# Performance work log

Measured on AMD Instinct MI355X. Metric: run time of the kernel, lower is better.

The kernel has to match this reference:

```python
import jax, jax.numpy as jnp
import numpy as np

N = 100000        # num nodes
E = 800000        # num edges
N_T = 1
IN_FEATS = 128
NUM_HEAD = 8
O_FEATS = 16
O_HEAD = NUM_HEAD * O_FEATS  # 128
LN_EPS = 1e-5


def setup_inputs() -> dict:
    key = jax.random.key(0)
    ks = [jax.random.fold_in(key, i) for i in range(16)]
    feats = jax.random.normal(ks[0], (N, N_T, IN_FEATS), dtype=jnp.float32)
    edge_src = jax.random.randint(ks[1], (E,), 0, N, dtype=jnp.int32)
    # ensure every node has at least one incoming edge (avoids 0/0 in wv/z)
    dst_rest = jax.random.randint(ks[2], (E - N,), 0, N, dtype=jnp.int32)
    edge_dst = jax.random.permutation(ks[3], jnp.concatenate([jnp.arange(N, dtype=jnp.int32), dst_rest]))
    s_in = 1.0 / np.sqrt(IN_FEATS)
    s_oh = 1.0 / np.sqrt(O_HEAD)
    Wq = jax.random.normal(ks[4], (IN_FEATS, O_HEAD), dtype=jnp.float32) * s_in
    bq = jnp.zeros((O_HEAD,), dtype=jnp.float32)
    Wk = jax.random.normal(ks[5], (IN_FEATS, O_HEAD), dtype=jnp.float32) * s_in
    bk = jnp.zeros((O_HEAD,), dtype=jnp.float32)
    Wv = jax.random.normal(ks[6], (IN_FEATS, O_HEAD), dtype=jnp.float32) * s_in
    bv = jnp.zeros((O_HEAD,), dtype=jnp.float32)
    Wo = jax.random.normal(ks[7], (O_HEAD, O_HEAD), dtype=jnp.float32) * s_oh
    bo = jnp.zeros((O_HEAD,), dtype=jnp.float32)
    Wffn = jax.random.normal(ks[8], (IN_FEATS, O_HEAD), dtype=jnp.float32) * s_in
    bffn = jnp.zeros((O_HEAD,), dtype=jnp.float32)
    ln_g = jnp.ones((O_HEAD,), dtype=jnp.float32)
    ln_b = jnp.zeros((O_HEAD,), dtype=jnp.float32)
    return {"feats": feats, "edge_src": edge_src, "edge_dst": edge_dst,
            "Wq": Wq, "bq": bq, "Wk": Wk, "bk": bk, "Wv": Wv, "bv": bv,
            "Wo": Wo, "bo": bo, "Wffn": Wffn, "bffn": bffn,
            "ln_g": ln_g, "ln_b": ln_b}


def _layer_norm(x, g, b):
    mu = jnp.mean(x, axis=-1, keepdims=True)
    var = jnp.mean(jnp.square(x - mu), axis=-1, keepdims=True)
    return (x - mu) * jax.lax.rsqrt(var + LN_EPS) * g + b


def reference(feats, edge_src, edge_dst, Wq, bq, Wk, bk, Wv, bv, Wo, bo, Wffn, bffn, ln_g, ln_b):
    n = feats.shape[0]
    # q/k/v projections: [N, n_T, H, D]
    q = (feats @ Wq + bq).reshape(n, N_T, NUM_HEAD, O_FEATS)
    k = (feats @ Wk + bk).reshape(n, N_T, NUM_HEAD, O_FEATS)
    v = (feats @ Wv + bv).reshape(n, N_T, NUM_HEAD, O_FEATS)
    # edge scores: src k . dst q, scaled, clamped exp  -> [E, n_T, H, 1]
    score = jnp.sum(k[edge_src] * q[edge_dst], axis=-1, keepdims=True)
    score = jnp.exp(jnp.clip(score / np.sqrt(IN_FEATS), -5.0, 5.0))
    # segment sums to destination nodes
    wv = jax.ops.segment_sum(v[edge_src] * score, edge_dst, num_segments=n)
    z = jax.ops.segment_sum(score, edge_dst, num_segments=n)
    wv = wv / z                                   # [N, n_T, H, D]
    o = wv.reshape(n, N_T, O_HEAD) @ Wo + bo      # output projection
    h = (feats @ Wffn + bffn) + o                 # FFN skip + attention out
    h = h + _layer_norm(h, ln_g, ln_b)
    return h
```

## Files before the change

kernel.cpp:

```cpp
#include <hip/hip_runtime.h>
#include <hip/hip_bf16.h>

#define N_NODES 100000
#define N_EDGES 800000
#define CAP     64
#define NTILES  ((N_NODES + 63) / 64)

typedef unsigned short u16;
typedef unsigned int   u32;
typedef __attribute__((ext_vector_type(8))) short bf16x8;
typedef __attribute__((ext_vector_type(4))) float f32x4;

__device__ inline u32 pack_bf2(float a, float b) {
    __hip_bfloat16 ha = __float2bfloat16(a), hb = __float2bfloat16(b);
    u16 ua, ub;
    __builtin_memcpy(&ua, &ha, 2);
    __builtin_memcpy(&ub, &hb, 2);
    return (u32)ua | ((u32)ub << 16);
}
__device__ inline u16 to_bf16(float a) {
    __hip_bfloat16 h = __float2bfloat16(a);
    u16 u; __builtin_memcpy(&u, &h, 2);
    return u;
}
__device__ inline void unpk(u32 w, float& a, float& b) {
    a = __uint_as_float(w << 16);
    b = __uint_as_float(w & 0xffff0000u);
}

__global__ __launch_bounds__(256) void prep_weights(
    const float* __restrict__ Wq, const float* __restrict__ Wk,
    const float* __restrict__ Wv, const float* __restrict__ Wf,
    const float* __restrict__ Wo, u16* __restrict__ WcatT, u16* __restrict__ WoT)
{
    int idx = blockIdx.x * 256 + threadIdx.x;
    if (idx < 512 * 128) {
        int n = idx >> 7, kk = idx & 127;
        const float* W = (n < 128) ? Wq : (n < 256) ? Wk : (n < 384) ? Wv : Wf;
        WcatT[idx] = to_bf16(W[kk * 128 + (n & 127)]);
    } else if (idx < 512 * 128 + 128 * 128) {
        int i2 = idx - 512 * 128;
        int n = i2 >> 7, kk = i2 & 127;
        WoT[i2] = to_bf16(Wo[kk * 128 + n]);
    }
}

__global__ __launch_bounds__(384, 3) void proj_mfma(
    const float* __restrict__ feats, const u16* __restrict__ WT,
    const float* __restrict__ bq, const float* __restrict__ bk,
    const float* __restrict__ bv,
    u16* __restrict__ q, u16* __restrict__ k, u16* __restrict__ v)
{
    __shared__ __align__(16) u16 As[64][136];
    const int tid = threadIdx.x;
    const int wid = tid >> 6, l = tid & 63;
    const int q4 = l >> 4, c16 = l & 15;
    const int colg0 = wid * 64;

    bf16x8 wfr[4][4];
    #pragma unroll
    for (int ks = 0; ks < 4; ++ks)
        #pragma unroll
        for (int nt = 0; nt < 4; ++nt)
            wfr[ks][nt] = *reinterpret_cast<const bf16x8*>(
                WT + (size_t)(colg0 + nt * 16 + c16) * 128 + ks * 32 + q4 * 8);

    const float* bias_src = (wid < 2) ? bq : (wid < 4) ? bk : bv;
    u16* outb = (wid < 2) ? q : (wid < 4) ? k : v;
    const int cbase = colg0 - (wid >> 1) * 128;

    for (int tile = blockIdx.x; tile < NTILES; tile += gridDim.x) {
        const int row0 = tile * 64;

        #pragma unroll
        for (int i = 0; i < 3; ++i) {
            int idx = tid + i * 384;
            if (idx < 1024) {
                int r = idx >> 4, c8 = (idx & 15) * 8;
                int gr = row0 + r;
                float4 f0, f1;
                if (gr < N_NODES) {
                    const float4* p = reinterpret_cast<const float4*>(feats + (size_t)gr * 128 + c8);
                    f0 = p[0]; f1 = p[1];
                } else {
                    f0 = make_float4(0.f,0.f,0.f,0.f); f1 = f0;
                }
                uint4 pk;
                pk.x = pack_bf2(f0.x, f0.y); pk.y = pack_bf2(f0.z, f0.w);
                pk.z = pack_bf2(f1.x, f1.y); pk.w = pack_bf2(f1.z, f1.w);
                *reinterpret_cast<uint4*>(&As[r][c8]) = pk;
            }
        }
        __syncthreads();

        f32x4 acc[4][4];
        #pragma unroll
        for (int a = 0; a < 4; ++a)
            #pragma unroll
            for (int b = 0; b < 4; ++b)
                acc[a][b] = (f32x4){0.f,0.f,0.f,0.f};

        #pragma unroll
        for (int ks = 0; ks < 4; ++ks) {
            const int k0 = ks * 32 + q4 * 8;
            bf16x8 afr[4];
            #pragma unroll
            for (int mt = 0; mt < 4; ++mt)
                afr[mt] = *reinterpret_cast<const bf16x8*>(&As[mt * 16 + c16][k0]);
            #pragma unroll
            for (int mt = 0; mt < 4; ++mt)
                #pragma unroll
                for (int nt = 0; nt < 4; ++nt)
                    acc[mt][nt] = __builtin_amdgcn_mfma_f32_16x16x32_bf16(
                        wfr[ks][nt], afr[mt], acc[mt][nt], 0, 0, 0);
        }

        #pragma unroll
        for (int nt = 0; nt < 4; ++nt) {
            const int c = cbase + nt * 16 + q4 * 4;
            float4 b4 = *reinterpret_cast<const float4*>(bias_src + c);
            #pragma unroll
            for (int mt = 0; mt < 4; ++mt) {
                int gr = row0 + mt * 16 + c16;
                if (gr < N_NODES) {
                    uint2 pk;
                    pk.x = pack_bf2(acc[mt][nt][0] + b4.x, acc[mt][nt][1] + b4.y);
                    pk.y = pack_bf2(acc[mt][nt][2] + b4.z, acc[mt][nt][3] + b4.w);
                    *reinterpret_cast<uint2*>(outb + (size_t)gr * 128 + c) = pk;
                }
            }
        }
        __syncthreads();
    }
}

__global__ __launch_bounds__(256) void bucket_kernel(
    const int* __restrict__ esrc, const int* __restrict__ edst,
    int* __restrict__ cnt, int* __restrict__ bucket)
{
    int e = blockIdx.x * 256 + threadIdx.x;
    if (e >= N_EDGES) return;
    int d = edst[e];
    int pos = atomicAdd(&cnt[d], 1);
    if (pos < CAP) bucket[(size_t)d * CAP + pos] = esrc[e];
}

__global__ __launch_bounds__(256) void agg_fused(
    const u16* __restrict__ q, const u16* __restrict__ k, const u16* __restrict__ v,
    const int* __restrict__ cnt, const int* __restrict__ bucket,
    u16* __restrict__ wv)
{
    const int wid  = threadIdx.x >> 6;
    const int lane = threadIdx.x & 63;
    const int node = blockIdx.x * 4 + wid;
    int deg = cnt[node]; if (deg > CAP) deg = CAP;

    const int grp = lane >> 3;
    const int el  = lane & 7;

    const float scale = 0.08838834764831845f;
    const uint4* qp = reinterpret_cast<const uint4*>(q + (size_t)node * 128 + el * 16);
    uint4 q0 = qp[0], q1 = qp[1];
    float qf[16];
    {
        u32 qw[8] = {q0.x,q0.y,q0.z,q0.w,q1.x,q1.y,q1.z,q1.w};
        #pragma unroll
        for (int j = 0; j < 8; ++j) {
            float a, b; unpk(qw[j], a, b);
            qf[2*j] = a * scale; qf[2*j+1] = b * scale;
        }
    }

    int srcs = (lane < deg) ? bucket[(size_t)node * CAP + lane] : 0;

    float acc[16];
    #pragma unroll
    for (int j = 0; j < 16; ++j) acc[j] = 0.f;
    float z = 0.f;

    const int nIter = (deg + 7) >> 3;
    for (int it = 0; it < nIter; ++it) {
        int i = it * 8 + grp;
        bool valid = (i < deg);
        int s = __shfl(srcs, i);
        const uint4* kp = reinterpret_cast<const uint4*>(k + (size_t)s * 128 + el * 16);
        uint4 k0 = kp[0], k1 = kp[1];
        const uint4* vp = reinterpret_cast<const uint4*>(v + (size_t)s * 128 + el * 16);
        uint4 v0 = vp[0], v1 = vp[1];

        u32 kw[8] = {k0.x,k0.y,k0.z,k0.w,k1.x,k1.y,k1.z,k1.w};
        float p = 0.f;
        #pragma unroll
        for (int j = 0; j < 8; ++j) {
            float a, b; unpk(kw[j], a, b);
            p = fmaf(a, qf[2*j], p);
            p = fmaf(b, qf[2*j+1], p);
        }
        p = fminf(fmaxf(p, -5.f), 5.f);
        float sc = valid ? __expf(p) : 0.f;

        u32 vw[8] = {v0.x,v0.y,v0.z,v0.w,v1.x,v1.y,v1.z,v1.w};
        #pragma unroll
        for (int j = 0; j < 8; ++j) {
            float a, b; unpk(vw[j], a, b);
            acc[2*j]   = fmaf(a, sc, acc[2*j]);
            acc[2*j+1] = fmaf(b, sc, acc[2*j+1]);
        }
        z += sc;
    }

    #pragma unroll
    for (int mask = 8; mask <= 32; mask <<= 1) {
        #pragma unroll
        for (int j = 0; j < 16; ++j) acc[j] += __shfl_xor(acc[j], mask);
        z += __shfl_xor(z, mask);
    }

    if (grp == 0) {
        float inv = 1.f / z;
        uint4 w0, w1;
        w0.x = pack_bf2(acc[0]*inv,  acc[1]*inv);
        w0.y = pack_bf2(acc[2]*inv,  acc[3]*inv);
        w0.z = pack_bf2(acc[4]*inv,  acc[5]*inv);
        w0.w = pack_bf2(acc[6]*inv,  acc[7]*inv);
        w1.x = pack_bf2(acc[8]*inv,  acc[9]*inv);
        w1.y = pack_bf2(acc[10]*inv, acc[11]*inv);
        w1.z = pack_bf2(acc[12]*inv, acc[13]*inv);
        w1.w = pack_bf2(acc[14]*inv, acc[15]*inv);
        uint4* wp = reinterpret_cast<uint4*>(wv + (size_t)node * 128 + el * 16);
        wp[0] = w0; wp[1] = w1;
    }
}

__global__ __launch_bounds__(256) void out_mfma(
    const float* __restrict__ feats, const u16* __restrict__ wv,
    const u16* __restrict__ WoT, const u16* __restrict__ WcatT,
    const float* __restrict__ bo, const float* __restrict__ bffn,
    const float* __restrict__ lg, const float* __restrict__ lb,
    float* __restrict__ out)
{
    __shared__ __align__(16) char smem[2 * 64 * 136 * sizeof(u16)];
    u16 (*Awv)[136] = reinterpret_cast<u16(*)[136]>(smem);
    u16 (*Aft)[136] = reinterpret_cast<u16(*)[136]>(smem + 64 * 136 * sizeof(u16));
    float (*Hs)[132] = reinterpret_cast<float(*)[132]>(smem);

    const int tid  = threadIdx.x;
    const int row0 = blockIdx.x * 64;
    const u16* WfT = WcatT + 384 * 128;

    #pragma unroll
    for (int i = 0; i < 4; ++i) {
        int idx = tid + i * 256;
        int r = idx >> 4, c8 = (idx & 15) * 8;
        int gr = row0 + r; if (gr >= N_NODES) gr = N_NODES - 1;
        *reinterpret_cast<uint4*>(&Awv[r][c8]) =
            *reinterpret_cast<const uint4*>(wv + (size_t)gr * 128 + c8);
        const float4* p = reinterpret_cast<const float4*>(feats + (size_t)gr * 128 + c8);
        float4 f0 = p[0], f1 = p[1];
        uint4 pk;
        pk.x = pack_bf2(f0.x, f0.y); pk.y = pack_bf2(f0.z, f0.w);
        pk.z = pack_bf2(f1.x, f1.y); pk.w = pack_bf2(f1.z, f1.w);
        *reinterpret_cast<uint4*>(&Aft[r][c8]) = pk;
    }
    __syncthreads();

    const int wid = tid >> 6, l = tid & 63;
    const int q4 = l >> 4, c16 = l & 15;
    const int col0 = wid * 32;

    f32x4 acc[4][2];
    #pragma unroll
    for (int a = 0; a < 4; ++a) { acc[a][0] = (f32x4){0.f,0.f,0.f,0.f}; acc[a][1] = acc[a][0]; }

    #pragma unroll
    for (int ks = 0; ks < 4; ++ks) {
        const int k0 = ks * 32 + q4 * 8;
        bf16x8 afr[4], bfr[2];
        #pragma unroll
        for (int mt = 0; mt < 4; ++mt)
            afr[mt] = *reinterpret_cast<const bf16x8*>(&Awv[mt * 16 + c16][k0]);
        #pragma unroll
        for (int nt = 0; nt < 2; ++nt)
            bfr[nt] = *reinterpret_cast<const bf16x8*>(WoT + (size_t)(col0 + nt * 16 + c16) * 128 + k0);
        #pragma unroll
        for (int mt = 0; mt < 4; ++mt)
            #pragma unroll
            for (int nt = 0; nt < 2; ++nt)
                acc[mt][nt] = __builtin_amdgcn_mfma_f32_16x16x32_bf16(afr[mt], bfr[nt], acc[mt][nt], 0, 0, 0);
    }
    #pragma unroll
    for (int ks = 0; ks < 4; ++ks) {
        const int k0 = ks * 32 + q4 * 8;
        bf16x8 afr[4], bfr[2];
        #pragma unroll
        for (int mt = 0; mt < 4; ++mt)
            afr[mt] = *reinterpret_cast<const bf16x8*>(&Aft[mt * 16 + c16][k0]);
        #pragma unroll
        for (int nt = 0; nt < 2; ++nt)
            bfr[nt] = *reinterpret_cast<const bf16x8*>(WfT + (size_t)(col0 + nt * 16 + c16) * 128 + k0);
        #pragma unroll
        for (int mt = 0; mt < 4; ++mt)
            #pragma unroll
            for (int nt = 0; nt < 2; ++nt)
                acc[mt][nt] = __builtin_amdgcn_mfma_f32_16x16x32_bf16(afr[mt], bfr[nt], acc[mt][nt], 0, 0, 0);
    }
    __syncthreads();

    #pragma unroll
    for (int nt = 0; nt < 2; ++nt) {
        const int col = col0 + nt * 16 + c16;
        const float bias = bo[col] + bffn[col];
        #pragma unroll
        for (int mt = 0; mt < 4; ++mt) {
            #pragma unroll
            for (int j = 0; j < 4; ++j) {
                int r = mt * 16 + q4 * 4 + j;
                Hs[r][col] = acc[mt][nt][j] + bias;
            }
        }
    }
    __syncthreads();

    const int r   = tid >> 2;
    const int sub = tid & 3;
    float sum = 0.f, sq = 0.f;
    #pragma unroll
    for (int jj = 0; jj < 8; ++jj) {
        float4 x = *reinterpret_cast<const float4*>(&Hs[r][(sub + jj * 4) * 4]);
        sum += x.x + x.y + x.z + x.w;
        sq  += x.x*x.x + x.y*x.y + x.z*x.z + x.w*x.w;
    }
    sum += __shfl_xor(sum, 1); sq += __shfl_xor(sq, 1);
    sum += __shfl_xor(sum, 2); sq += __shfl_xor(sq, 2);
    float mu   = sum * (1.f / 128.f);
    float var  = sq * (1.f / 128.f) - mu * mu;
    float rsig = rsqrtf(var + 1e-5f);

    int gr = row0 + r;
    if (gr < N_NODES) {
        #pragma unroll
        for (int jj = 0; jj < 8; ++jj) {
            int c = (sub + jj * 4) * 4;
            float4 x = *reinterpret_cast<const float4*>(&Hs[r][c]);
            float4 g = *reinterpret_cast<const float4*>(lg + c);
            float4 b = *reinterpret_cast<const float4*>(lb + c);
            float4 o;
            o.x = x.x + (x.x - mu) * rsig * g.x + b.x;
            o.y = x.y + (x.y - mu) * rsig * g.y + b.y;
            o.z = x.z + (x.z - mu) * rsig * g.z + b.z;
            o.w = x.w + (x.w - mu) * rsig * g.w + b.w;
            *reinterpret_cast<float4*>(out + (size_t)gr * 128 + c) = o;
        }
    }
}

extern "C" void kernel_launch(void* const* d_in, const int* in_sizes, int n_in,
                              void* d_out, int out_size, void* d_ws, size_t ws_size,
                              hipStream_t stream) {
    const float* feats = (const float*)d_in[0];
    const int*   esrc  = (const int*)d_in[1];
    const int*   edst  = (const int*)d_in[2];
    const float* Wq = (const float*)d_in[3];  const float* bq = (const float*)d_in[4];
    const float* Wk = (const float*)d_in[5];  const float* bk = (const float*)d_in[6];
    const float* Wv = (const float*)d_in[7];  const float* bv = (const float*)d_in[8];
    const float* Wo = (const float*)d_in[9];  const float* bo = (const float*)d_in[10];
    const float* Wf = (const float*)d_in[11]; const float* bf = (const float*)d_in[12];
    const float* lg = (const float*)d_in[13]; const float* lb = (const float*)d_in[14];
    float* out = (float*)d_out;

    char* ws = (char*)d_ws;
    const size_t NB = (size_t)N_NODES * 128 * sizeof(u16);
    u16* q     = (u16*)(ws);
    u16* k     = (u16*)(ws + NB);
    u16* v     = (u16*)(ws + 2 * NB);
    u16* wv    = (u16*)(ws + 3 * NB);
    u16* WcatT = (u16*)(ws + 4 * NB);
    u16* WoT   = (u16*)(ws + 4 * NB + 512 * 128 * sizeof(u16));
    int* cnt   = (int*)(ws + 4 * NB + (512 * 128 + 128 * 128) * sizeof(u16));
    int* bucket= (int*)(ws + 4 * NB + (512 * 128 + 128 * 128) * sizeof(u16)
                             + (size_t)N_NODES * sizeof(int));

    hipMemsetAsync(cnt, 0, (size_t)N_NODES * sizeof(int), stream);

    prep_weights<<<320, 256, 0, stream>>>(Wq, Wk, Wv, Wf, Wo, WcatT, WoT);
    proj_mfma<<<521, 384, 0, stream>>>(feats, WcatT, bq, bk, bv, q, k, v);
    bucket_kernel<<<(N_EDGES + 255) / 256, 256, 0, stream>>>(esrc, edst, cnt, bucket);
    agg_fused<<<N_NODES / 4, 256, 0, stream>>>(q, k, v, cnt, bucket, wv);
    out_mfma<<<(N_NODES + 63) / 64, 256, 0, stream>>>(feats, wv, WoT, WcatT,
                                                      bo, bf, lg, lb, out);
}
```

Measured before the change: 220.0 us.

## Load projection A-fragments directly from global memory, drop LDS staging and persistent loop

The QKV projection kernel no longer stages the 64-row feats tile into shared memory. Each lane now loads its own fp32 feats slice, converts it to bf16 and packs it straight into MFMA A-fragments. The grid-stride persistent loop is replaced by one block per tile (NTILES blocks), which removes the __syncthreads barriers and the LDS footprint. In exchange, each of the 6 waves independently re-reads the same feats rows from global memory/cache, giving 6x redundant global traffic and conversion work, while the per-block weight fragment load is no longer amortized over several tiles.

New measurement: 244.0 us. 10.9% more time.

```diff
diff --git a/kernel.cpp b/kernel.cpp
--- a/kernel.cpp
+++ b/kernel.cpp
@@ -51,7 +51,6 @@
     const float* __restrict__ bv,
     u16* __restrict__ q, u16* __restrict__ k, u16* __restrict__ v)
 {
-    __shared__ __align__(16) u16 As[64][136];
     const int tid = threadIdx.x;
     const int wid = tid >> 6, l = tid & 63;
     const int q4 = l >> 4, c16 = l & 15;
@@ -69,68 +68,56 @@
     u16* outb = (wid < 2) ? q : (wid < 4) ? k : v;
     const int cbase = colg0 - (wid >> 1) * 128;
 
-    for (int tile = blockIdx.x; tile < NTILES; tile += gridDim.x) {
-        const int row0 = tile * 64;
-
-        #pragma unroll
-        for (int i = 0; i < 3; ++i) {
-            int idx = tid + i * 384;
-            if (idx < 1024) {
-                int r = idx >> 4, c8 = (idx & 15) * 8;
-                int gr = row0 + r;
-                float4 f0, f1;
-                if (gr < N_NODES) {
-                    const float4* p = reinterpret_cast<const float4*>(feats + (size_t)gr * 128 + c8);
-                    f0 = p[0]; f1 = p[1];
-                } else {
-                    f0 = make_float4(0.f,0.f,0.f,0.f); f1 = f0;
-                }
-                uint4 pk;
-                pk.x = pack_bf2(f0.x, f0.y); pk.y = pack_bf2(f0.z, f0.w);
-                pk.z = pack_bf2(f1.x, f1.y); pk.w = pack_bf2(f1.z, f1.w);
-                *reinterpret_cast<uint4*>(&As[r][c8]) = pk;
+    const int row0 = blockIdx.x * 64;
+    const float* arow[4];
+    #pragma unroll
+    for (int mt = 0; mt < 4; ++mt) {
+        int gr = row0 + mt * 16 + c16;
+        arow[mt] = feats + (size_t)(gr < N_NODES ? gr : N_NODES - 1) * 128;
+    }
+
+    f32x4 acc[4][4];
+    #pragma unroll
+    for (int a = 0; a < 4; ++a)
+        #pragma unroll
+        for (int b = 0; b < 4; ++b)
+            acc[a][b] = (f32x4){0.f,0.f,0.f,0.f};
+
+    #pragma unroll
+    for (int ks = 0; ks < 4; ++ks) {
+        const int col = ks * 32 + q4 * 8;
+        bf16x8 afr[4];
+        #pragma unroll
+        for (int mt = 0; mt < 4; ++mt) {
+            const float4* p = reinterpret_cast<const float4*>(arow[mt] + col);
+            float4 f0 = p[0], f1 = p[1];
+            u32 u0 = pack_bf2(f0.x, f0.y), u1 = pack_bf2(f0.z, f0.w);
+            u32 u2 = pack_bf2(f1.x, f1.y), u3 = pack_bf2(f1.z, f1.w);
+            uint4 pk; pk.x=u0; pk.y=u1; pk.z=u2; pk.w=u3;
+            afr[mt] = *reinterpret_cast<bf16x8*>(&pk);
+        }
+        #pragma unroll
+        for (int mt = 0; mt < 4; ++mt)
+            #pragma unroll
+            for (int nt = 0; nt < 4; ++nt)
+                acc[mt][nt] = __builtin_amdgcn_mfma_f32_16x16x32_bf16(
+                    wfr[ks][nt], afr[mt], acc[mt][nt], 0, 0, 0);
+    }
+
+    #pragma unroll
+    for (int nt = 0; nt < 4; ++nt) {
+        const int c = cbase + nt * 16 + q4 * 4;
+        float4 b4 = *reinterpret_cast<const float4*>(bias_src + c);
+        #pragma unroll
+        for (int mt = 0; mt < 4; ++mt) {
+            int gr = row0 + mt * 16 + c16;
+            if (gr < N_NODES) {
+                uint2 pk;
+                pk.x = pack_bf2(acc[mt][nt][0] + b4.x, acc[mt][nt][1] + b4.y);
+                pk.y = pack_bf2(acc[mt][nt][2] + b4.z, acc[mt][nt][3] + b4.w);
+                *reinterpret_cast<uint2*>(outb + (size_t)gr * 128 + c) = pk;
             }
         }
-        __syncthreads();
-
-        f32x4 acc[4][4];
-        #pragma unroll
-        for (int a = 0; a < 4; ++a)
-            #pragma unroll
-            for (int b = 0; b < 4; ++b)
-                acc[a][b] = (f32x4){0.f,0.f,0.f,0.f};
-
-        #pragma unroll
-        for (int ks = 0; ks < 4; ++ks) {
-            const int k0 = ks * 32 + q4 * 8;
-            bf16x8 afr[4];
-            #pragma unroll
-            for (int mt = 0; mt < 4; ++mt)
-                afr[mt] = *reinterpret_cast<const bf16x8*>(&As[mt * 16 + c16][k0]);
-            #pragma unroll
-            for (int mt = 0; mt < 4; ++mt)
-                #pragma unroll
-                for (int nt = 0; nt < 4; ++nt)
-                    acc[mt][nt] = __builtin_amdgcn_mfma_f32_16x16x32_bf16(
-                        wfr[ks][nt], afr[mt], acc[mt][nt], 0, 0, 0);
-        }
-
-        #pragma unroll
-        for (int nt = 0; nt < 4; ++nt) {
-            const int c = cbase + nt * 16 + q4 * 4;
-            float4 b4 = *reinterpret_cast<const float4*>(bias_src + c);
-            #pragma unroll
-            for (int mt = 0; mt < 4; ++mt) {
-                int gr = row0 + mt * 16 + c16;
-                if (gr < N_NODES) {
-                    uint2 pk;
-                    pk.x = pack_bf2(acc[mt][nt][0] + b4.x, acc[mt][nt][1] + b4.y);
-                    pk.y = pack_bf2(acc[mt][nt][2] + b4.z, acc[mt][nt][3] + b4.w);
-                    *reinterpret_cast<uint2*>(outb + (size_t)gr * 128 + c) = pk;
-                }
-            }
-        }
-        __syncthreads();
     }
 }
 
@@ -383,7 +370,7 @@
     hipMemsetAsync(cnt, 0, (size_t)N_NODES * sizeof(int), stream);
 
     prep_weights<<<320, 256, 0, stream>>>(Wq, Wk, Wv, Wf, Wo, WcatT, WoT);
-    proj_mfma<<<521, 384, 0, stream>>>(feats, WcatT, bq, bk, bv, q, k, v);
+    proj_mfma<<<NTILES, 384, 0, stream>>>(feats, WcatT, bq, bk, bv, q, k, v);
     bucket_kernel<<<(N_EDGES + 255) / 256, 256, 0, stream>>>(esrc, edst, cnt, bucket);
     agg_fused<<<N_NODES / 4, 256, 0, stream>>>(q, k, v, cnt, bucket, wv);
     out_mfma<<<(N_NODES + 63) / 64, 256, 0, stream>>>(feats, wv, WoT, WcatT,
```

## Fuse edge bucketing into projection kernel and coalesce layernorm output stores

Applied to the files above, without the earlier changes.

The separate bucket kernel is folded into the tail of the projection kernel as a grid-stride loop, and the projection grid is doubled so more blocks share the projection tiles and the edge work. This removes one launch and lets the atomic bucketing overlap with projection blocks that are still running. The layernorm epilogue now writes per-row mean and rstd to shared memory and then stores output with consecutive threads covering consecutive columns, so global writes are coalesced. The cost is an extra barrier, and the larger projection grid loads the weight fragments into registers in more blocks.

Result: faster. 195.2 us (-11.3%).

```diff
diff --git a/kernel.cpp b/kernel.cpp
--- a/kernel.cpp
+++ b/kernel.cpp
@@ -5,6 +5,7 @@
 #define N_EDGES 800000
 #define CAP     64
 #define NTILES  ((N_NODES + 63) / 64)
+#define PROJ_BLOCKS 1042
 
 typedef unsigned short u16;
 typedef unsigned int   u32;
@@ -49,7 +50,9 @@
     const float* __restrict__ feats, const u16* __restrict__ WT,
     const float* __restrict__ bq, const float* __restrict__ bk,
     const float* __restrict__ bv,
-    u16* __restrict__ q, u16* __restrict__ k, u16* __restrict__ v)
+    u16* __restrict__ q, u16* __restrict__ k, u16* __restrict__ v,
+    const int* __restrict__ esrc, const int* __restrict__ edst,
+    int* __restrict__ cnt, int* __restrict__ bucket)
 {
     __shared__ __align__(16) u16 As[64][136];
     const int tid = threadIdx.x;
@@ -132,17 +135,12 @@
         }
         __syncthreads();
     }
-}
-
-__global__ __launch_bounds__(256) void bucket_kernel(
-    const int* __restrict__ esrc, const int* __restrict__ edst,
-    int* __restrict__ cnt, int* __restrict__ bucket)
-{
-    int e = blockIdx.x * 256 + threadIdx.x;
-    if (e >= N_EDGES) return;
-    int d = edst[e];
-    int pos = atomicAdd(&cnt[d], 1);
-    if (pos < CAP) bucket[(size_t)d * CAP + pos] = esrc[e];
+
+    for (int e = blockIdx.x * 384 + tid; e < N_EDGES; e += gridDim.x * 384) {
+        int d = edst[e];
+        int pos = atomicAdd(&cnt[d], 1);
+        if (pos < CAP) bucket[(size_t)d * CAP + pos] = esrc[e];
+    }
 }
 
 __global__ __launch_bounds__(256) void agg_fused(
@@ -243,6 +241,8 @@
     u16 (*Awv)[136] = reinterpret_cast<u16(*)[136]>(smem);
     u16 (*Aft)[136] = reinterpret_cast<u16(*)[136]>(smem + 64 * 136 * sizeof(u16));
     float (*Hs)[132] = reinterpret_cast<float(*)[132]>(smem);
+    float* muS = reinterpret_cast<float*>(smem + 64 * 132 * sizeof(float));
+    float* rsS = muS + 64;
 
     const int tid  = threadIdx.x;
     const int row0 = blockIdx.x * 64;
@@ -321,35 +321,40 @@
     }
     __syncthreads();
 
-    const int r   = tid >> 2;
-    const int sub = tid & 3;
-    float sum = 0.f, sq = 0.f;
-    #pragma unroll
-    for (int jj = 0; jj < 8; ++jj) {
-        float4 x = *reinterpret_cast<const float4*>(&Hs[r][(sub + jj * 4) * 4]);
-        sum += x.x + x.y + x.z + x.w;
-        sq  += x.x*x.x + x.y*x.y + x.z*x.z + x.w*x.w;
-    }
-    sum += __shfl_xor(sum, 1); sq += __shfl_xor(sq, 1);
-    sum += __shfl_xor(sum, 2); sq += __shfl_xor(sq, 2);
-    float mu   = sum * (1.f / 128.f);
-    float var  = sq * (1.f / 128.f) - mu * mu;
-    float rsig = rsqrtf(var + 1e-5f);
-
-    int gr = row0 + r;
-    if (gr < N_NODES) {
+    {
+        const int r   = tid >> 2;
+        const int sub = tid & 3;
+        float sum = 0.f, sq = 0.f;
         #pragma unroll
         for (int jj = 0; jj < 8; ++jj) {
-            int c = (sub + jj * 4) * 4;
-            float4 x = *reinterpret_cast<const float4*>(&Hs[r][c]);
-            float4 g = *reinterpret_cast<const float4*>(lg + c);
-            float4 b = *reinterpret_cast<const float4*>(lb + c);
+            float4 x = *reinterpret_cast<const float4*>(&Hs[r][(sub + jj * 4) * 4]);
+            sum += x.x + x.y + x.z + x.w;
+            sq  += x.x*x.x + x.y*x.y + x.z*x.z + x.w*x.w;
+        }
+        sum += __shfl_xor(sum, 1); sq += __shfl_xor(sq, 1);
+        sum += __shfl_xor(sum, 2); sq += __shfl_xor(sq, 2);
+        float mu   = sum * (1.f / 128.f);
+        float var  = sq * (1.f / 128.f) - mu * mu;
+        if (sub == 0) { muS[r] = mu; rsS[r] = rsqrtf(var + 1e-5f); }
+    }
+    __syncthreads();
+
+    #pragma unroll
+    for (int i = 0; i < 8; ++i) {
+        int idx = i * 256 + tid;
+        int rr = idx >> 5, c4 = idx & 31;
+        int gr = row0 + rr;
+        if (gr < N_NODES) {
+            float4 x = *reinterpret_cast<const float4*>(&Hs[rr][c4 * 4]);
+            float4 g = *reinterpret_cast<const float4*>(lg + c4 * 4);
+            float4 b = *reinterpret_cast<const float4*>(lb + c4 * 4);
+            float m = muS[rr], rs = rsS[rr];
             float4 o;
-            o.x = x.x + (x.x - mu) * rsig * g.x + b.x;
-            o.y = x.y + (x.y - mu) * rsig * g.y + b.y;
-            o.z = x.z + (x.z - mu) * rsig * g.z + b.z;
-            o.w = x.w + (x.w - mu) * rsig * g.w + b.w;
-            *reinterpret_cast<float4*>(out + (size_t)gr * 128 + c) = o;
+            o.x = x.x + (x.x - m) * rs * g.x + b.x;
+            o.y = x.y + (x.y - m) * rs * g.y + b.y;
+            o.z = x.z + (x.z - m) * rs * g.z + b.z;
+            o.w = x.w + (x.w - m) * rs * g.w + b.w;
+            *reinterpret_cast<float4*>(out + (size_t)gr * 128 + c4 * 4) = o;
         }
     }
 }
@@ -383,8 +388,8 @@
     hipMemsetAsync(cnt, 0, (size_t)N_NODES * sizeof(int), stream);
 
     prep_weights<<<320, 256, 0, stream>>>(Wq, Wk, Wv, Wf, Wo, WcatT, WoT);
-    proj_mfma<<<521, 384, 0, stream>>>(feats, WcatT, bq, bk, bv, q, k, v);
-    bucket_kernel<<<(N_EDGES + 255) / 256, 256, 0, stream>>>(esrc, edst, cnt, bucket);
+    proj_mfma<<<PROJ_BLOCKS, 384, 0, stream>>>(feats, WcatT, bq, bk, bv, q, k, v,
+                                               esrc, edst, cnt, bucket);
     agg_fused<<<N_NODES / 4, 256, 0, stream>>>(q, k, v, cnt, bucket, wv);
     out_mfma<<<(N_NODES + 63) / 64, 256, 0, stream>>>(feats, wv, WoT, WcatT,
                                                       bo, bf, lg, lb, out);
```
